# Optimization experiments

Hardware: AMD Instinct MI355X
Metric: run time of the kernel (lower is better)

The kernel has to match this reference:

```python
import jax, jax.numpy as jnp
import numpy as np

NUM_ROWS = 16384
H = 2048
K = 4
EXPERT_NUM = 64


def setup_inputs() -> dict:
    key = jax.random.key(0)
    k1, k2, k3 = jax.random.split(key, 3)
    x = jax.random.normal(k1, (NUM_ROWS, H), dtype=jnp.float32)
    expert_idx = jax.random.randint(k2, (NUM_ROWS, K), 0, EXPERT_NUM, dtype=jnp.int32)
    scale = jax.random.uniform(k3, (NUM_ROWS,), dtype=jnp.float32)
    return {"x": x, "expert_idx": expert_idx, "scale": scale, "expert_num": EXPERT_NUM}


def reference(x, expert_idx, scale, expert_num):
    # Dropless MoE token routing (drop_pad_mode=0, active_num=0 -> all tokens,
    # quant_mode=-1 with scale, expert_tokens_num_type=1, full active range).
    num_rows, h = x.shape
    k = expert_idx.shape[-1]
    n = num_rows * k
    eidx = expert_idx.reshape(-1)                     # [n]
    sorted_idx = jnp.argsort(eidx, stable=True)       # stable sort by expert id
    src_row = sorted_idx // k                         # original token row per expanded slot
    expanded_x = x[src_row]                           # [n, h] gathered tokens, expert-grouped
    # inverse permutation: position of each original (row,k) slot in the expanded output
    expanded_row_idx = jnp.zeros((n,), dtype=jnp.int32).at[sorted_idx].set(
        jnp.arange(n, dtype=jnp.int32))
    expert_tokens_count = jnp.bincount(eidx, length=expert_num).astype(jnp.int32)
    expanded_scale = scale[src_row].astype(jnp.float32)  # [n]
    return expanded_x, expanded_row_idx, expert_tokens_count, expanded_scale
```

## Files before the change

### kernel.cpp

```cpp
#include <hip/hip_runtime.h>

#define NROWS   16384
#define HDIM    2048
#define TOPK    4
#define NEXP    64
#define NSLOT   (NROWS * TOPK)
#define SLOTS_PER_BLOCK 256
#define NBLK    (NSLOT / SLOTS_PER_BLOCK)
#define CHUNK   16
#define NCHUNK  (NBLK / CHUNK)

typedef float f4 __attribute__((ext_vector_type(4)));

__global__ void hist_kernel(const int* __restrict__ eidx, int* __restrict__ hist) {
    __shared__ int h[NEXP];
    int t = threadIdx.x;
    if (t < NEXP) h[t] = 0;
    __syncthreads();
    int slot = blockIdx.x * SLOTS_PER_BLOCK + t;
    int e = eidx[slot];
    atomicAdd(&h[e], 1);
    __syncthreads();
    if (t < NEXP) hist[blockIdx.x * NEXP + t] = h[t];
}

__global__ void __launch_bounds__(1024) scan_kernel(const int* __restrict__ hist,
                                                    int* __restrict__ base,
                                                    float* __restrict__ out_counts) {
    __shared__ int partial[NCHUNK][NEXP];
    __shared__ int expert_off[NEXP];
    int tid = threadIdx.x;
    int c = tid >> 6;
    int e = tid & 63;
    int b0 = c * CHUNK;

    int s = 0;
    #pragma unroll
    for (int i = 0; i < CHUNK; ++i) s += hist[(b0 + i) * NEXP + e];
    partial[c][e] = s;
    __syncthreads();

    int excl = 0;
    #pragma unroll
    for (int i = 0; i < NCHUNK; ++i) {
        int v = partial[i][e];
        excl += (i < c) ? v : 0;
    }

    if (tid < 64) {
        int total = 0;
        #pragma unroll
        for (int i = 0; i < NCHUNK; ++i) total += partial[i][tid];
        out_counts[tid] = (float)total;
        int incl = total;
        #pragma unroll
        for (int d = 1; d < 64; d <<= 1) {
            int y = __shfl_up(incl, d, 64);
            if (tid >= d) incl += y;
        }
        expert_off[tid] = incl - total;
    }
    __syncthreads();

    int running = expert_off[e] + excl;
    #pragma unroll
    for (int i = 0; i < CHUNK; ++i) {
        int idx = (b0 + i) * NEXP + e;
        base[idx] = running;
        running += hist[idx];
    }
}

__global__ void rank_kernel(const int* __restrict__ eidx, const int* __restrict__ base,
                            const float* __restrict__ scale,
                            int* __restrict__ dest_ws, float* __restrict__ out_idx,
                            float* __restrict__ out_scale) {
    __shared__ int se[SLOTS_PER_BLOCK];
    int t = threadIdx.x;
    int slot = blockIdx.x * SLOTS_PER_BLOCK + t;
    int e = eidx[slot];
    se[t] = e;
    __syncthreads();
    int rank = 0;
    #pragma unroll 8
    for (int i = 0; i < SLOTS_PER_BLOCK; ++i) {
        int v = se[i];
        rank += (i < t && v == e) ? 1 : 0;
    }
    int dest = base[blockIdx.x * NEXP + e] + rank;
    dest_ws[slot] = dest;
    out_idx[slot] = (float)dest;
    out_scale[dest] = scale[slot >> 2];
}

__global__ void __launch_bounds__(256) copy_kernel(const f4* __restrict__ x,
                                                   const int* __restrict__ dest_ws,
                                                   f4* __restrict__ out) {
    int row = blockIdx.x;
    int t = threadIdx.x;
    const f4* xs = x + (size_t)row * (HDIM / 4);
    f4 v0 = __builtin_nontemporal_load(xs + t);
    f4 v1 = __builtin_nontemporal_load(xs + t + 256);
    const int4 d = *reinterpret_cast<const int4*>(dest_ws + ((size_t)row << 2));
    f4* o0 = out + (size_t)d.x * (HDIM / 4);
    f4* o1 = out + (size_t)d.y * (HDIM / 4);
    f4* o2 = out + (size_t)d.z * (HDIM / 4);
    f4* o3 = out + (size_t)d.w * (HDIM / 4);
    __builtin_nontemporal_store(v0, o0 + t);
    __builtin_nontemporal_store(v1, o0 + t + 256);
    __builtin_nontemporal_store(v0, o1 + t);
    __builtin_nontemporal_store(v1, o1 + t + 256);
    __builtin_nontemporal_store(v0, o2 + t);
    __builtin_nontemporal_store(v1, o2 + t + 256);
    __builtin_nontemporal_store(v0, o3 + t);
    __builtin_nontemporal_store(v1, o3 + t + 256);
}

extern "C" void kernel_launch(void* const* d_in, const int* in_sizes, int n_in,
                              void* d_out, int out_size, void* d_ws, size_t ws_size,
                              hipStream_t stream) {
    const float* x     = (const float*)d_in[0];
    const int*   eidx  = (const int*)d_in[1];
    const float* scale = (const float*)d_in[2];

    float* out        = (float*)d_out;
    float* out_x      = out;
    float* out_idx    = out + (size_t)NSLOT * HDIM;
    float* out_counts = out_idx + NSLOT;
    float* out_scale  = out_counts + NEXP;

    int* hist = (int*)d_ws;
    int* base = hist + NBLK * NEXP;
    int* dest = base + NBLK * NEXP;

    hist_kernel<<<NBLK, SLOTS_PER_BLOCK, 0, stream>>>(eidx, hist);
    scan_kernel<<<1, 1024, 0, stream>>>(hist, base, out_counts);
    rank_kernel<<<NBLK, SLOTS_PER_BLOCK, 0, stream>>>(eidx, base, scale,
                                                      dest, out_idx, out_scale);
    copy_kernel<<<NROWS, 256, 0, stream>>>((const f4*)x, dest, (f4*)out_x);
}
```

Measured before the change: 637.5 us.

## Fuse rank computation into histogram kernel and destination resolution into copy kernel

```diff
diff --git a/kernel.cpp b/kernel.cpp
--- a/kernel.cpp
+++ b/kernel.cpp
@@ -12,14 +12,26 @@
 
 typedef float f4 __attribute__((ext_vector_type(4)));
 
-__global__ void hist_kernel(const int* __restrict__ eidx, int* __restrict__ hist) {
+__global__ void hist_rank_kernel(const int* __restrict__ eidx,
+                                 int* __restrict__ hist,
+                                 int* __restrict__ packed) {
+    __shared__ int se[SLOTS_PER_BLOCK];
     __shared__ int h[NEXP];
     int t = threadIdx.x;
     if (t < NEXP) h[t] = 0;
-    __syncthreads();
     int slot = blockIdx.x * SLOTS_PER_BLOCK + t;
     int e = eidx[slot];
-    atomicAdd(&h[e], 1);
+    se[t] = e;
+    __syncthreads();
+    int rank = 0, cnt = 0;
+    #pragma unroll 8
+    for (int i = 0; i < SLOTS_PER_BLOCK; ++i) {
+        int m = (se[i] == e);
+        cnt  += m;
+        rank += (i < t) ? m : 0;
+    }
+    packed[slot] = (e << 16) | rank;
+    if (rank == 0) h[e] = cnt;
     __syncthreads();
     if (t < NEXP) hist[blockIdx.x * NEXP + t] = h[t];
 }
@@ -71,41 +83,45 @@
     }
 }
 
-__global__ void rank_kernel(const int* __restrict__ eidx, const int* __restrict__ base,
-                            const float* __restrict__ scale,
-                            int* __restrict__ dest_ws, float* __restrict__ out_idx,
-                            float* __restrict__ out_scale) {
-    __shared__ int se[SLOTS_PER_BLOCK];
-    int t = threadIdx.x;
-    int slot = blockIdx.x * SLOTS_PER_BLOCK + t;
-    int e = eidx[slot];
-    se[t] = e;
-    __syncthreads();
-    int rank = 0;
-    #pragma unroll 8
-    for (int i = 0; i < SLOTS_PER_BLOCK; ++i) {
-        int v = se[i];
-        rank += (i < t && v == e) ? 1 : 0;
-    }
-    int dest = base[blockIdx.x * NEXP + e] + rank;
-    dest_ws[slot] = dest;
-    out_idx[slot] = (float)dest;
-    out_scale[dest] = scale[slot >> 2];
-}
-
 __global__ void __launch_bounds__(256) copy_kernel(const f4* __restrict__ x,
-                                                   const int* __restrict__ dest_ws,
+                                                   const int* __restrict__ packed,
+                                                   const int* __restrict__ base,
+                                                   const float* __restrict__ scale,
+                                                   float* __restrict__ out_idx,
+                                                   float* __restrict__ out_scale,
                                                    f4* __restrict__ out) {
     int row = blockIdx.x;
     int t = threadIdx.x;
     const f4* xs = x + (size_t)row * (HDIM / 4);
     f4 v0 = __builtin_nontemporal_load(xs + t);
     f4 v1 = __builtin_nontemporal_load(xs + t + 256);
-    const int4 d = *reinterpret_cast<const int4*>(dest_ws + ((size_t)row << 2));
-    f4* o0 = out + (size_t)d.x * (HDIM / 4);
-    f4* o1 = out + (size_t)d.y * (HDIM / 4);
-    f4* o2 = out + (size_t)d.z * (HDIM / 4);
-    f4* o3 = out + (size_t)d.w * (HDIM / 4);
+
+    int slot0 = row << 2;
+    int b     = row >> 6;
+    const int* bb = base + b * NEXP;
+    int p0 = packed[slot0 + 0];
+    int p1 = packed[slot0 + 1];
+    int p2 = packed[slot0 + 2];
+    int p3 = packed[slot0 + 3];
+    int d0 = bb[p0 >> 16] + (p0 & 0xffff);
+    int d1 = bb[p1 >> 16] + (p1 & 0xffff);
+    int d2 = bb[p2 >> 16] + (p2 & 0xffff);
+    int d3 = bb[p3 >> 16] + (p3 & 0xffff);
+
+    if (t == 0) {
+        f4 idx = {(float)d0, (float)d1, (float)d2, (float)d3};
+        *reinterpret_cast<f4*>(out_idx + slot0) = idx;
+        float sc = scale[row];
+        out_scale[d0] = sc;
+        out_scale[d1] = sc;
+        out_scale[d2] = sc;
+        out_scale[d3] = sc;
+    }
+
+    f4* o0 = out + (size_t)d0 * (HDIM / 4);
+    f4* o1 = out + (size_t)d1 * (HDIM / 4);
+    f4* o2 = out + (size_t)d2 * (HDIM / 4);
+    f4* o3 = out + (size_t)d3 * (HDIM / 4);
     __builtin_nontemporal_store(v0, o0 + t);
     __builtin_nontemporal_store(v1, o0 + t + 256);
     __builtin_nontemporal_store(v0, o1 + t);
@@ -129,13 +145,12 @@
     float* out_counts = out_idx + NSLOT;
     float* out_scale  = out_counts + NEXP;
 
-    int* hist = (int*)d_ws;
-    int* base = hist + NBLK * NEXP;
-    int* dest = base + NBLK * NEXP;
+    int* hist   = (int*)d_ws;
+    int* base   = hist + NBLK * NEXP;
+    int* packed = base + NBLK * NEXP;
 
-    hist_kernel<<<NBLK, SLOTS_PER_BLOCK, 0, stream>>>(eidx, hist);
+    hist_rank_kernel<<<NBLK, SLOTS_PER_BLOCK, 0, stream>>>(eidx, hist, packed);
     scan_kernel<<<1, 1024, 0, stream>>>(hist, base, out_counts);
-    rank_kernel<<<NBLK, SLOTS_PER_BLOCK, 0, stream>>>(eidx, base, scale,
-                                                      dest, out_idx, out_scale);
-    copy_kernel<<<NROWS, 256, 0, stream>>>((const f4*)x, dest, (f4*)out_x);
+    copy_kernel<<<NROWS, 256, 0, stream>>>((const f4*)x, packed, base, scale,
+                                           out_idx, out_scale, (f4*)out_x);
 }
```

New measurement: 629.2 us (median of 2 runs). No clear change (-1.3%).
